# Kernel tuning notes

Hardware: AMD Instinct MI355X
Metric: run time of the kernel (lower is better)

The kernel has to match this reference:

```python
import jax, jax.numpy as jnp
import numpy as np
from math import factorial

NODES = 40000      # number of nodes
EDGES = 640000     # number of edges (avg degree 16)
MUL = 8            # multiplicity of each irrep in hidden (8x0e+8x1e+8x2e)
NB = 16            # radial basis size (radial_neurons[0])
MAXR = 3.0         # max_radius
NSPECIES = 8
DEG = 16.0         # num_neighbors normalization
R8 = 1.0 / np.sqrt(8.0)

# ---------- real Clebsch-Gordan coefficients (precomputed with numpy) ----------
def _clebsch(j1, m1, j2, m2, j3, m3):
    f = factorial
    if m1 + m2 != m3:
        return 0.0
    pref = ((2*j3+1) * f(j3+j1-j2) * f(j3-j1+j2) * f(j1+j2-j3) / f(j1+j2+j3+1)) ** 0.5
    pref *= (f(j3+m3)*f(j3-m3)*f(j1-m1)*f(j1+m1)*f(j2-m2)*f(j2+m2)) ** 0.5
    lo = max(0, j2-j3-m1, j1-j3+m2)
    hi = min(j1+j2-j3, j1-m1, j2+m2)
    s = 0.0
    for k in range(lo, hi+1):
        s += (-1)**k / (f(k)*f(j1+j2-j3-k)*f(j1-m1-k)*f(j2+m2-k)*f(j3-j2+m1+k)*f(j3-j1-m2+k))
    return pref * s

def _U(l):
    # complex -> real spherical-harmonic change of basis (rows: real m, cols: complex m)
    U = np.zeros((2*l+1, 2*l+1), dtype=complex)
    s2 = 2 ** -0.5
    for m in range(-l, l+1):
        if m > 0:
            U[m+l, m+l] = (-1)**m * s2; U[m+l, -m+l] = s2
        elif m == 0:
            U[l, l] = 1.0
        else:
            U[m+l, m+l] = 1j*s2; U[m+l, -m+l] = -1j*((-1)**m)*s2
    return U

def _real_cg(l1, l2, l3):
    C = np.zeros((2*l1+1, 2*l2+1, 2*l3+1))
    for m1 in range(-l1, l1+1):
        for m2 in range(-l2, l2+1):
            m3 = m1 + m2
            if abs(m3) <= l3:
                C[m1+l1, m2+l2, m3+l3] = _clebsch(l1, m1, l2, m2, l3, m3)
    T = np.einsum('am,bn,co,mno->abc', _U(l1).conj(), _U(l2).conj(), _U(l3), C)
    R = T.imag if np.abs(T.imag).max() > np.abs(T.real).max() else T.real
    return jnp.asarray(R.astype(np.float32))

PATHS = [(0,0,0),(0,1,1),(0,2,2),(1,0,1),(1,1,0),(1,1,1),(1,1,2),
         (1,2,1),(1,2,2),(2,0,2),(2,1,1),(2,1,2),(2,2,0),(2,2,1),(2,2,2)]
CG = {p: _real_cg(*p) for p in PATHS}
NIN = {0: 3.0, 1: 6.0, 2: 6.0}  # fan-in path counts per output l in hidden convs

# ---------- irrep feature layout: [.., 72] = 8x0e | 8x1e | 8x2e ----------
def _split(h):
    lead = h.shape[:-1]
    return (h[..., :MUL],
            h[..., MUL:4*MUL].reshape(lead + (MUL, 3)),
            h[..., 4*MUL:].reshape(lead + (MUL, 5)))

def _merge(s, v, t):
    lead = s.shape[:-1]
    return jnp.concatenate([s, v.reshape(lead + (3*MUL,)), t.reshape(lead + (5*MUL,))], -1)

def _act(h):
    # e3nn Activation: silu on 0e scalars, identity on l>0
    s, v, t = _split(h)
    return _merge(jax.nn.silu(s), v, t)

def _radial(emb, w1, b1, w2, b2):
    return jax.nn.silu(emb @ w1 + b1) @ w2 + b2

def _sh(u):
    # component-normalized real spherical harmonics l=0,1,2 of unit vectors u [E,3]
    x, y, z = u[:, 0], u[:, 1], u[:, 2]
    c15 = np.sqrt(15.0); c5 = np.sqrt(5.0); c3 = np.sqrt(3.0)
    y1 = jnp.stack([y, z, x], -1) * c3
    y2 = jnp.stack([c15*x*y, c15*y*z, 0.5*c5*(3*z*z - 1.0), c15*x*z, 0.5*c15*(x*x - y*y)], -1)
    return jnp.concatenate([jnp.ones_like(x)[:, None], y1, y2], -1)

def _soft_onehot(r):
    # e3nn soft_one_hot_linspace, basis='smooth_finite', cutoff=True
    values = jnp.linspace(0.0, MAXR, NB + 2)[1:-1]
    step = MAXR / (NB + 1)
    d = (r[:, None] - values) / step
    inside = jnp.abs(d) < 1.0
    dd = jnp.where(inside, d, 0.0)
    f = jnp.exp(-1.0 / (1.0 + dd)) * jnp.exp(-1.0 / (1.0 - dd))
    return 1.14136 * np.exp(2.0) * jnp.where(inside, f, 0.0)

def _tp_first(hs, sh, w):
    # uvu TP: 8x0e (x) SH(1x0e+1x1e+1x2e) -> hidden; hs [E,8], sh [E,9], w [E,3,8]
    m_s = w[:, 0] * hs * sh[:, :1]
    m_v = w[:, 1][..., None] * hs[..., None] * sh[:, None, 1:4]
    m_t = w[:, 2][..., None] * hs[..., None] * sh[:, None, 4:9]
    return _merge(m_s, m_v, m_t)

def _tp_uuu(h1, h2, w):
    # depthwise (uuu) CG tensor product hidden (x) hidden -> hidden; w [E,15,8]
    s1, v1, t1 = _split(h1); s2, v2, t2 = _split(h2)
    a = {0: s1[..., None], 1: v1, 2: t1}
    b = {0: s2[..., None], 1: v2, 2: t2}
    out = {0: 0.0, 1: 0.0, 2: 0.0}
    for p, (l1, l2, l3) in enumerate(PATHS):
        out[l3] = out[l3] + w[:, p, :, None] * jnp.einsum('eci,ecj,ijk->eck', a[l1], b[l2], CG[(l1, l2, l3)])
    return _merge(out[0][..., 0] / np.sqrt(NIN[0]), out[1] / np.sqrt(NIN[1]), out[2] / np.sqrt(NIN[2]))

def _lin_hidden(h, lin):
    # irrep-wise linear self-connection, lin [3,8,8]
    s, v, t = _split(h)
    return _merge(s @ lin[0] * R8,
                  jnp.einsum('ncm,cd->ndm', v, lin[1]) * R8,
                  jnp.einsum('ncm,cd->ndm', t, lin[2]) * R8)

def _model(x, edge_index, edge_vec, embed_w, lin0, lin1, lin2, out_w,
           r0_w1, r0_b1, r0_w2, r0_b2, r1_w1, r1_b1, r1_w2, r1_b2,
           r2_w1, r2_b1, r2_w2, r2_b2):
    src, dst = edge_index[0], edge_index[1]
    h = embed_w[x]                                   # [N, 8] scalar node feats
    r = jnp.sqrt(jnp.sum(edge_vec**2, -1) + 1e-12)
    emb = _soft_onehot(r)                            # [E, 16]
    hb_sh = _sh(edge_vec / r[:, None])               # [E, 9]
    rdeg = 1.0 / np.sqrt(DEG)
    # conv 0 + activation
    w = _radial(emb, r0_w1, r0_b1, r0_w2, r0_b2).reshape(-1, 3, MUL)
    m = _tp_first(h[src], hb_sh, w)                  # [E, 72]
    agg = jax.ops.segment_sum(m, dst, num_segments=NODES) * rdeg
    h = _act(agg.at[:, :MUL].add((h @ lin0) * R8))
    hb = _act(m)
    # convs 1..2 + activation
    for (w1, b1, w2, b2, lin) in ((r1_w1, r1_b1, r1_w2, r1_b2, lin1),
                                  (r2_w1, r2_b1, r2_w2, r2_b2, lin2)):
        w = _radial(emb, w1, b1, w2, b2).reshape(-1, 15, MUL)
        m = _tp_uuu(h[src], hb, w)
        agg = jax.ops.segment_sum(m, dst, num_segments=NODES) * rdeg
        h = _act(_lin_hidden(h, lin) + agg)
        hb = _act(m)
    # output FullyConnectedTensorProduct(h, h) -> 8x0e (paths l(x)l->0)
    s, v, t = _split(h)
    i0 = s[:, :, None] * s[:, None, :]
    i1 = jnp.einsum('nim,njm->nij', v, v) / np.sqrt(3.0)
    i2 = jnp.einsum('nim,njm->nij', t, t) / np.sqrt(5.0)
    out = (jnp.einsum('nij,ijk->nk', i0, out_w[0])
           + jnp.einsum('nij,ijk->nk', i1, out_w[1])
           + jnp.einsum('nij,ijk->nk', i2, out_w[2])) / np.sqrt(3.0 * MUL * MUL)
    return out

def setup_inputs() -> dict:
    key = jax.random.key(0)
    ks = jax.random.split(key, 16)
    inp = {}
    inp['x'] = jax.random.randint(ks[0], (NODES,), 0, NSPECIES)
    inp['edge_index'] = jax.random.randint(ks[1], (2, EDGES), 0, NODES)
    inp['edge_vec'] = jax.random.normal(ks[2], (EDGES, 3), dtype=jnp.float32)
    inp['embed_w'] = jax.random.normal(ks[3], (NSPECIES, MUL), dtype=jnp.float32)
    inp['lin0'] = jax.random.normal(ks[4], (MUL, MUL), dtype=jnp.float32)
    inp['lin1'] = jax.random.normal(ks[5], (3, MUL, MUL), dtype=jnp.float32)
    inp['lin2'] = jax.random.normal(ks[6], (3, MUL, MUL), dtype=jnp.float32)
    inp['out_w'] = jax.random.normal(ks[7], (3, MUL, MUL, MUL), dtype=jnp.float32)
    for i, (name, od) in enumerate((('r0', 3*MUL), ('r1', 15*MUL), ('r2', 15*MUL))):
        k1, k2 = jax.random.split(ks[8+i])
        inp[name+'_w1'] = jax.random.normal(k1, (NB, 64), dtype=jnp.float32) / np.sqrt(NB)
        inp[name+'_b1'] = jnp.zeros((64,), dtype=jnp.float32)
        inp[name+'_w2'] = jax.random.normal(k2, (64, od), dtype=jnp.float32) / 8.0
        inp[name+'_b2'] = jnp.zeros((od,), dtype=jnp.float32)
    return inp

def reference(x, edge_index, edge_vec, embed_w, lin0, lin1, lin2, out_w,
              r0_w1, r0_b1, r0_w2, r0_b2, r1_w1, r1_b1, r1_w2, r1_b2,
              r2_w1, r2_b1, r2_w2, r2_b2):
    return _model(x, edge_index, edge_vec, embed_w, lin0, lin1, lin2, out_w,
                  r0_w1, r0_b1, r0_w2, r0_b2, r1_w1, r1_b1, r1_w2, r1_b2,
                  r2_w1, r2_b1, r2_w2, r2_b2)
```

## Files before the change

kernel.cpp:

```cpp
#include <hip/hip_runtime.h>

#define NODES 40000
#define EDGES 640000

typedef float f32x2v __attribute__((ext_vector_type(2)));
typedef float f32x4v __attribute__((ext_vector_type(4)));
typedef short short8v __attribute__((ext_vector_type(8)));

__device__ __forceinline__ float silu_f(float x) { return x / (1.0f + __expf(-x)); }
__device__ __forceinline__ f32x2v mk2(float a, float b) { f32x2v r; r[0] = a; r[1] = b; return r; }

__device__ __forceinline__ void tp_uuu2(const f32x2v* wv,
                                        f32x2v as, const f32x2v* av, const f32x2v* at,
                                        f32x2v bs, const f32x2v* bv, const f32x2v* bt,
                                        f32x2v& ms, f32x2v* mv, f32x2v* mt)
{
    const float CR = 0.70710678f;
    const float K1 = 0.31622777f;
    const float K3 = 0.54772256f;
    const float KA = 0.40824829f;
    const float KB = 0.70710678f;
    const float KC = 0.81649658f;
    const float L4 = 0.63245553f;
    const float G2 = 0.53452248f;
    const float G1 = 0.26726124f;
    const float HH = 0.46291005f;

    f32x2v os = {0.f, 0.f};
    f32x2v ov0 = {0.f, 0.f}, ov1 = {0.f, 0.f}, ov2 = {0.f, 0.f};
    f32x2v ot0 = {0.f, 0.f}, ot1 = {0.f, 0.f}, ot2 = {0.f, 0.f};
    f32x2v ot3 = {0.f, 0.f}, ot4 = {0.f, 0.f};

    os += wv[0] * as * bs;
    ov0 += wv[1] * as * bv[0]; ov1 += wv[1] * as * bv[1]; ov2 += wv[1] * as * bv[2];
    ot0 += wv[2] * as * bt[0]; ot1 += wv[2] * as * bt[1]; ot2 += wv[2] * as * bt[2];
    ot3 += wv[2] * as * bt[3]; ot4 += wv[2] * as * bt[4];
    ov0 += wv[3] * av[0] * bs; ov1 += wv[3] * av[1] * bs; ov2 += wv[3] * av[2] * bs;
    os += wv[4] * (-0.57735027f) * (av[0]*bv[0] + av[1]*bv[1] + av[2]*bv[2]);
    ov0 += wv[5] * CR * (av[1]*bv[2] - av[2]*bv[1]);
    ov1 += wv[5] * CR * (av[2]*bv[0] - av[0]*bv[2]);
    ov2 += wv[5] * CR * (av[0]*bv[1] - av[1]*bv[0]);
    ot0 += wv[6] * CR * (av[2]*bv[0] + av[0]*bv[2]);
    ot1 += wv[6] * CR * (av[0]*bv[1] + av[1]*bv[0]);
    ot2 += wv[6] * 0.40824829f * (2.f*av[1]*bv[1] - av[2]*bv[2] - av[0]*bv[0]);
    ot3 += wv[6] * CR * (av[2]*bv[1] + av[1]*bv[2]);
    ot4 += wv[6] * CR * (av[2]*bv[2] - av[0]*bv[0]);
    ov0 += wv[7] * (-K3*av[1]*bt[1] + K1*av[0]*bt[2] - K3*av[2]*bt[0] + K3*av[0]*bt[4]);
    ov1 += wv[7] * (-2.f*K1*av[1]*bt[2] - K3*av[2]*bt[3] - K3*av[0]*bt[1]);
    ov2 += wv[7] * (-K3*av[1]*bt[3] + K1*av[2]*bt[2] - K3*av[0]*bt[0] - K3*av[2]*bt[4]);
    ot0 += wv[8] * ( KC*av[1]*bt[4] - KA*av[2]*bt[3] + KA*av[0]*bt[1]);
    ot1 += wv[8] * ( KA*av[1]*bt[3] - KB*av[2]*bt[2] - KA*av[0]*bt[0] - KA*av[2]*bt[4]);
    ot2 += wv[8] * ( KB*av[2]*bt[1] - KB*av[0]*bt[3]);
    ot3 += wv[8] * (-KA*av[1]*bt[1] + KB*av[0]*bt[2] + KA*av[2]*bt[0] - KA*av[0]*bt[4]);
    ot4 += wv[8] * (-KC*av[1]*bt[0] + KA*av[2]*bt[1] + KA*av[0]*bt[3]);
    ot0 += wv[9] * at[0] * bs; ot1 += wv[9] * at[1] * bs; ot2 += wv[9] * at[2] * bs;
    ot3 += wv[9] * at[3] * bs; ot4 += wv[9] * at[4] * bs;
    ov0 += wv[10] * (-K3*bv[1]*at[1] + K1*bv[0]*at[2] - K3*bv[2]*at[0] + K3*bv[0]*at[4]);
    ov1 += wv[10] * (-2.f*K1*bv[1]*at[2] - K3*bv[2]*at[3] - K3*bv[0]*at[1]);
    ov2 += wv[10] * (-K3*bv[1]*at[3] + K1*bv[2]*at[2] - K3*bv[0]*at[0] - K3*bv[2]*at[4]);
    ot0 -= wv[11] * ( KC*bv[1]*at[4] - KA*bv[2]*at[3] + KA*bv[0]*at[1]);
    ot1 -= wv[11] * ( KA*bv[1]*at[3] - KB*bv[2]*at[2] - KA*bv[0]*at[0] - KA*bv[2]*at[4]);
    ot2 -= wv[11] * ( KB*bv[2]*at[1] - KB*bv[0]*at[3]);
    ot3 -= wv[11] * (-KA*bv[1]*at[1] + KB*bv[0]*at[2] + KA*bv[2]*at[0] - KA*bv[0]*at[4]);
    ot4 -= wv[11] * (-KC*bv[1]*at[0] + KA*bv[2]*at[1] + KA*bv[0]*at[3]);
    os += wv[12] * 0.44721360f * (at[0]*bt[0] + at[1]*bt[1] + at[2]*bt[2] + at[3]*bt[3] + at[4]*bt[4]);
    ov0 += wv[13] * ( K1*(at[0]*bt[1] - at[1]*bt[0]) + K3*(at[3]*bt[2] - at[2]*bt[3]) + K1*(at[4]*bt[3] - at[3]*bt[4]) );
    ov1 += wv[13] * ( L4*(at[0]*bt[4] - at[4]*bt[0]) + K1*(at[1]*bt[3] - at[3]*bt[1]) );
    ov2 += wv[13] * ( K1*(at[3]*bt[0] - at[0]*bt[3]) + K3*(at[2]*bt[1] - at[1]*bt[2]) + K1*(at[4]*bt[1] - at[1]*bt[4]) );
    ot0 += wv[14] * ( G2*(at[2]*bt[0] + at[0]*bt[2]) - HH*(at[1]*bt[3] + at[3]*bt[1]) );
    ot1 += wv[14] * (-HH*(at[3]*bt[0] + at[0]*bt[3]) + HH*(at[1]*bt[4] + at[4]*bt[1]) - G1*(at[2]*bt[1] + at[1]*bt[2]) );
    ot2 += wv[14] * ( G2*(at[0]*bt[0] + at[4]*bt[4] - at[2]*bt[2]) - G1*(at[1]*bt[1] + at[3]*bt[3]) );
    ot3 += wv[14] * (-HH*(at[1]*bt[0] + at[0]*bt[1]) - HH*(at[3]*bt[4] + at[4]*bt[3]) - G1*(at[2]*bt[3] + at[3]*bt[2]) );
    ot4 += wv[14] * ( G2*(at[2]*bt[4] + at[4]*bt[2]) + HH*(at[1]*bt[1] - at[3]*bt[3]) );

    ms = os * 0.57735027f;
    mv[0] = ov0 * 0.40824829f; mv[1] = ov1 * 0.40824829f; mv[2] = ov2 * 0.40824829f;
    mt[0] = ot0 * 0.40824829f; mt[1] = ot1 * 0.40824829f; mt[2] = ot2 * 0.40824829f;
    mt[3] = ot3 * 0.40824829f; mt[4] = ot4 * 0.40824829f;
}

__global__ void deg_kernel(const int* __restrict__ eidx, int* __restrict__ deg)
{
    int e = blockIdx.x * 256 + threadIdx.x;
    if (e < EDGES) atomicAdd(&deg[eidx[EDGES + e]], 1);
}

__launch_bounds__(1024)
__global__ void scan_kernel(const int* __restrict__ deg, int* __restrict__ off,
                            int* __restrict__ cursor)
{
    __shared__ int part[1024];
    const int t = threadIdx.x;
    const int base = t * 40;
    int v[40];
    if (t < 1000) {
        const int4* p4 = (const int4*)(deg + base);
        #pragma unroll
        for (int i = 0; i < 10; ++i) {
            int4 q = p4[i];
            v[4 * i + 0] = q.x; v[4 * i + 1] = q.y;
            v[4 * i + 2] = q.z; v[4 * i + 3] = q.w;
        }
    } else {
        #pragma unroll
        for (int i = 0; i < 40; ++i) v[i] = 0;
    }
    int loc[40];
    int s = 0;
    #pragma unroll
    for (int i = 0; i < 40; ++i) { loc[i] = s; s += v[i]; }
    part[t] = s;
    __syncthreads();
    for (int d = 1; d < 1024; d <<= 1) {
        int vv = (t >= d) ? part[t - d] : 0;
        __syncthreads();
        part[t] += vv;
        __syncthreads();
    }
    int tb = (t == 0) ? 0 : part[t - 1];
    if (t < 1000) {
        #pragma unroll
        for (int i = 0; i < 40; ++i) {
            off[base + i] = tb + loc[i];
            cursor[base + i] = tb + loc[i];
        }
    }
    if (t == 1023) off[NODES] = part[1023];
}

__global__ void build_kernel(const int* __restrict__ eidx, const float* __restrict__ ev,
                             int* __restrict__ cursor,
                             float* __restrict__ evp, int* __restrict__ srcs)
{
    int e = blockIdx.x * 256 + threadIdx.x;
    if (e < EDGES) {
        int dst = eidx[EDGES + e];
        int p = atomicAdd(&cursor[dst], 1);
        srcs[p] = eidx[e];
        evp[p * 3 + 0] = ev[e * 3 + 0];
        evp[p * 3 + 1] = ev[e * 3 + 1];
        evp[p * 3 + 2] = ev[e * 3 + 2];
    }
}

__launch_bounds__(256, 3)
__global__ void layer0_edge(const float* __restrict__ evp, const int* __restrict__ srcs,
                            const int* __restrict__ xs, const float* __restrict__ embw,
                            const float* __restrict__ w1, const float* __restrict__ b1,
                            const float* __restrict__ w2, const float* __restrict__ b2,
                            float* __restrict__ mbuf)
{
    __shared__ float emb_s[128 * 17];
    __shared__ float hid_s[128 * 68];
    __shared__ float w2t[24 * 68];
    const int tid = threadIdx.x;
    const int e0 = blockIdx.x * 128;

    for (int idx = tid; idx < 64 * 24; idx += 256) {
        int j = idx / 24, o = idx - j * 24;
        w2t[o * 68 + j] = w2[idx];
    }
    for (int idx = tid; idx < 2048; idx += 256) {
        int e = idx >> 4, i = idx & 15;
        const float* ep = evp + (size_t)(e0 + e) * 3;
        float ex = ep[0], ey = ep[1], ez = ep[2];
        float r = sqrtf(ex * ex + ey * ey + ez * ez + 1e-12f);
        float d = r * (17.0f / 3.0f) - (float)(i + 1);
        float f = 0.0f;
        if (fabsf(d) < 1.0f) f = 8.433572869f * __expf(-2.0f / (1.0f - d * d));
        emb_s[e * 17 + i] = f;
    }
    __syncthreads();

    {
        const int egp = tid >> 3;
        const int jb = (tid & 7) * 8;
        float acc2[4][8];
        #pragma unroll
        for (int el = 0; el < 4; ++el)
            #pragma unroll
            for (int k = 0; k < 8; ++k) acc2[el][k] = b1[jb + k];
        #pragma unroll
        for (int i = 0; i < 16; ++i) {
            float4 wa = *(const float4*)&w1[i * 64 + jb];
            float4 wb = *(const float4*)&w1[i * 64 + jb + 4];
            #pragma unroll
            for (int el = 0; el < 4; ++el) {
                float evv = emb_s[(egp * 4 + el) * 17 + i];
                acc2[el][0] += evv * wa.x; acc2[el][1] += evv * wa.y;
                acc2[el][2] += evv * wa.z; acc2[el][3] += evv * wa.w;
                acc2[el][4] += evv * wb.x; acc2[el][5] += evv * wb.y;
                acc2[el][6] += evv * wb.z; acc2[el][7] += evv * wb.w;
            }
        }
        #pragma unroll
        for (int el = 0; el < 4; ++el)
            #pragma unroll
            for (int k = 0; k < 8; ++k)
                hid_s[(egp * 4 + el) * 68 + jb + k] = silu_f(acc2[el][k]);
    }
    __syncthreads();

    const int c = tid & 7, g = (tid >> 3) & 7, wv_ = tid >> 6;
    float wacc[3][4];
    #pragma unroll
    for (int p = 0; p < 3; ++p) {
        float bb = b2[p * 8 + c];
        #pragma unroll
        for (int q = 0; q < 4; ++q) wacc[p][q] = bb;
    }
    for (int jb = 0; jb < 64; jb += 4) {
        float4 h4[4];
        #pragma unroll
        for (int q = 0; q < 4; ++q)
            h4[q] = *(const float4*)&hid_s[(wv_ * 32 + q * 8 + g) * 68 + jb];
        #pragma unroll
        for (int p = 0; p < 3; ++p) {
            float4 w4 = *(const float4*)&w2t[(p * 8 + c) * 68 + jb];
            #pragma unroll
            for (int q = 0; q < 4; ++q)
                wacc[p][q] += h4[q].x * w4.x + h4[q].y * w4.y + h4[q].z * w4.z + h4[q].w * w4.w;
        }
    }

    const int ebase = wv_ * 32 + g;
    const float c3 = 1.7320508f, c15 = 3.8729833f, c5 = 2.2360680f;
    #pragma unroll
    for (int q = 0; q < 4; ++q) {
        const int sl = e0 + ebase + 8 * q;
        const int sn = srcs[sl];
        float hs = embw[xs[sn] * 8 + c];
        const float* ep = evp + (size_t)sl * 3;
        float ex = ep[0], ey = ep[1], ez = ep[2];
        float r = sqrtf(ex * ex + ey * ey + ez * ez + 1e-12f);
        float inv = 1.0f / r;
        float x = ex * inv, y = ey * inv, z = ez * inv;

        float* me = mbuf + (size_t)sl * 72 + c * 9;
        me[0] = wacc[0][q] * hs;
        me[1] = wacc[1][q] * hs * (c3 * y);
        me[2] = wacc[1][q] * hs * (c3 * z);
        me[3] = wacc[1][q] * hs * (c3 * x);
        me[4] = wacc[2][q] * hs * (c15 * x * y);
        me[5] = wacc[2][q] * hs * (c15 * y * z);
        me[6] = wacc[2][q] * hs * (0.5f * c5 * (3.f * z * z - 1.f));
        me[7] = wacc[2][q] * hs * (c15 * x * z);
        me[8] = wacc[2][q] * hs * (0.5f * c15 * (x * x - y * y));
    }
}

__launch_bounds__(256, 2)
__global__ void tp_edge(const float* __restrict__ evp, const int* __restrict__ srcs,
                        const float* __restrict__ h,
                        const float* __restrict__ w1, const float* __restrict__ b1,
                        const float* __restrict__ w2, const float* __restrict__ b2,
                        float* __restrict__ mbuf)
{
    __shared__ float ws_t[120 * 132];
    __shared__ unsigned short hid_s[128 * 64];
    float* emb_s = ws_t;

    const int tid = threadIdx.x;
    const int e0 = blockIdx.x * 128;

    for (int idx = tid; idx < 2048; idx += 256) {
        int e = idx >> 4, i = idx & 15;
        const float* ep = evp + (size_t)(e0 + e) * 3;
        float ex = ep[0], ey = ep[1], ez = ep[2];
        float r = sqrtf(ex * ex + ey * ey + ez * ez + 1e-12f);
        float d = r * (17.0f / 3.0f) - (float)(i + 1);
        float f = 0.0f;
        if (fabsf(d) < 1.0f) f = 8.433572869f * __expf(-2.0f / (1.0f - d * d));
        emb_s[e * 17 + i] = f;
    }
    __syncthreads();

    {
        const int egp = tid >> 3;
        const int jb = (tid & 7) * 8;
        f32x2v acc2[2][8];
        #pragma unroll
        for (int pr = 0; pr < 2; ++pr)
            #pragma unroll
            for (int k = 0; k < 8; ++k) { float bb = b1[jb + k]; acc2[pr][k] = mk2(bb, bb); }
        #pragma unroll
        for (int i = 0; i < 16; ++i) {
            float4 wa = *(const float4*)&w1[i * 64 + jb];
            float4 wb = *(const float4*)&w1[i * 64 + jb + 4];
            #pragma unroll
            for (int pr = 0; pr < 2; ++pr) {
                f32x2v evv = mk2(emb_s[(egp * 4 + 2 * pr) * 17 + i],
                                 emb_s[(egp * 4 + 2 * pr + 1) * 17 + i]);
                acc2[pr][0] += evv * wa.x; acc2[pr][1] += evv * wa.y;
                acc2[pr][2] += evv * wa.z; acc2[pr][3] += evv * wa.w;
                acc2[pr][4] += evv * wb.x; acc2[pr][5] += evv * wb.y;
                acc2[pr][6] += evv * wb.z; acc2[pr][7] += evv * wb.w;
            }
        }
        #pragma unroll
        for (int pr = 0; pr < 2; ++pr) {
            #pragma unroll
            for (int u = 0; u < 2; ++u) {
                unsigned int us[8];
                #pragma unroll
                for (int k = 0; k < 8; ++k) {
                    unsigned int b = __float_as_uint(silu_f(acc2[pr][k][u]));
                    b += 0x7fffu + ((b >> 16) & 1u);
                    us[k] = b >> 16;
                }
                uint4 pk;
                pk.x = us[0] | (us[1] << 16);
                pk.y = us[2] | (us[3] << 16);
                pk.z = us[4] | (us[5] << 16);
                pk.w = us[6] | (us[7] << 16);
                int rr = egp * 4 + 2 * pr + u;
                *(uint4*)&hid_s[rr * 64 + (jb ^ ((rr & 7) << 3))] = pk;
            }
        }
    }
    __syncthreads();

    {
        const int l  = tid & 63;
        const int wq = tid >> 6;
        const int lr = l & 15;
        const int lg = l >> 4;

        short8v bhi[2][2], blo[2][2];
        #pragma unroll
        for (int n2 = 0; n2 < 2; ++n2) {
            int col  = (2 * wq + n2) * 16 + lr;
            int colc = col < 120 ? col : 119;
            #pragma unroll
            for (int ks = 0; ks < 2; ++ks) {
                short8v hv, lv;
                #pragma unroll
                for (int j = 0; j < 8; ++j) {
                    int k = ks * 32 + lg * 8 + j;
                    float v = w2[k * 120 + colc];
                    if (col >= 120) v = 0.0f;
                    unsigned bb = __float_as_uint(v);
                    unsigned rh = bb + 0x7fffu + ((bb >> 16) & 1u);
                    float hf = __uint_as_float((rh >> 16) << 16);
                    unsigned bl = __float_as_uint(v - hf);
                    bl += 0x7fffu + ((bl >> 16) & 1u);
                    hv[j] = (short)(rh >> 16);
                    lv[j] = (short)(bl >> 16);
                }
                bhi[n2][ks] = hv;
                blo[n2][ks] = lv;
            }
        }

        for (int m = 0; m < 8; ++m) {
            int e  = 16 * m + lr;
            int sw = (e & 7) << 3;
            short8v a0 = *(const short8v*)&hid_s[e * 64 + ((lg * 8) ^ sw)];
            short8v a1 = *(const short8v*)&hid_s[e * 64 + ((32 + lg * 8) ^ sw)];
            #pragma unroll
            for (int n2 = 0; n2 < 2; ++n2) {
                int col = (2 * wq + n2) * 16 + lr;
                float bias = (col < 120) ? b2[col] : 0.0f;
                f32x4v acc;
                acc[0] = bias; acc[1] = bias; acc[2] = bias; acc[3] = bias;
                acc = __builtin_amdgcn_mfma_f32_16x16x32_bf16(a0, bhi[n2][0], acc, 0, 0, 0);
                acc = __builtin_amdgcn_mfma_f32_16x16x32_bf16(a1, bhi[n2][1], acc, 0, 0, 0);
                acc = __builtin_amdgcn_mfma_f32_16x16x32_bf16(a0, blo[n2][0], acc, 0, 0, 0);
                acc = __builtin_amdgcn_mfma_f32_16x16x32_bf16(a1, blo[n2][1], acc, 0, 0, 0);
                if (col < 120)
                    *(f32x4v*)&ws_t[col * 132 + 16 * m + lg * 4] = acc;
            }
        }
    }
    __syncthreads();

    const int c = tid & 7, g = (tid >> 3) & 7, wv_ = tid >> 6;
    const int ebase = wv_ * 32 + g;
    int sn[4];
    #pragma unroll
    for (int q = 0; q < 4; ++q) sn[q] = srcs[e0 + ebase + 8 * q];

    #pragma unroll
    for (int hh = 0; hh < 2; ++hh) {
        const float* hn0 = h + (size_t)sn[2 * hh] * 72 + c * 9;
        const float* hn1 = h + (size_t)sn[2 * hh + 1] * 72 + c * 9;
        const float* me0 = mbuf + (size_t)(e0 + ebase + 8 * (2 * hh)) * 72 + c * 9;
        const float* me1 = mbuf + (size_t)(e0 + ebase + 8 * (2 * hh + 1)) * 72 + c * 9;

        f32x2v as = mk2(hn0[0], hn1[0]);
        f32x2v av[3], at[5], bv[3], bt[5];
        #pragma unroll
        for (int i = 0; i < 3; ++i) av[i] = mk2(hn0[1 + i], hn1[1 + i]);
        #pragma unroll
        for (int i = 0; i < 5; ++i) at[i] = mk2(hn0[4 + i], hn1[4 + i]);
        f32x2v bs = mk2(silu_f(me0[0]), silu_f(me1[0]));
        #pragma unroll
        for (int i = 0; i < 3; ++i) bv[i] = mk2(me0[1 + i], me1[1 + i]);
        #pragma unroll
        for (int i = 0; i < 5; ++i) bt[i] = mk2(me0[4 + i], me1[4 + i]);

        f32x2v wvv[15];
        #pragma unroll
        for (int p = 0; p < 15; ++p)
            wvv[p] = mk2(ws_t[(p * 8 + c) * 132 + ebase + 16 * hh],
                         ws_t[(p * 8 + c) * 132 + ebase + 16 * hh + 8]);

        f32x2v ms, mv[3], mt[5];
        tp_uuu2(wvv, as, av, at, bs, bv, bt, ms, mv, mt);

        float* mo0 = mbuf + (size_t)(e0 + ebase + 8 * (2 * hh)) * 72 + c * 9;
        float* mo1 = mbuf + (size_t)(e0 + ebase + 8 * (2 * hh + 1)) * 72 + c * 9;
        mo0[0] = ms[0]; mo1[0] = ms[1];
        #pragma unroll
        for (int i = 0; i < 3; ++i) { mo0[1 + i] = mv[i][0]; mo1[1 + i] = mv[i][1]; }
        #pragma unroll
        for (int i = 0; i < 5; ++i) { mo0[4 + i] = mt[i][0]; mo1[4 + i] = mt[i][1]; }
    }
}

__global__ void node0(const int* __restrict__ xs, const float* __restrict__ embw,
                      const float* __restrict__ lin0, const float* __restrict__ mbuf,
                      const int* __restrict__ off, float* __restrict__ h)
{
    int idx = blockIdx.x * 256 + threadIdx.x;
    int n = idx >> 3, c = idx & 7;
    int xb = xs[n] * 8;
    float dot = 0.f;
    #pragma unroll
    for (int d = 0; d < 8; ++d) dot += embw[xb + d] * lin0[d * 8 + c];

    float an[9];
    #pragma unroll
    for (int i = 0; i < 9; ++i) an[i] = 0.f;
    const int beg = off[n], end = off[n + 1];
    for (int p = beg; p < end; ++p) {
        const float* me = mbuf + (size_t)p * 72 + c * 9;
        #pragma unroll
        for (int i = 0; i < 9; ++i) an[i] += me[i];
    }

    float* hn = h + (size_t)n * 72 + c * 9;
    hn[0] = silu_f(an[0] * 0.25f + dot * 0.35355339f);
    #pragma unroll
    for (int i = 1; i < 9; ++i) hn[i] = an[i] * 0.25f;
}

__global__ void node12(const float* __restrict__ hin, const float* __restrict__ lin,
                       const float* __restrict__ mbuf, const int* __restrict__ off,
                       float* __restrict__ hout)
{
    int idx = blockIdx.x * 256 + threadIdx.x;
    int n = idx >> 3, d = idx & 7;

    float an[9];
    #pragma unroll
    for (int i = 0; i < 9; ++i) an[i] = 0.f;
    const int beg = off[n], end = off[n + 1];
    for (int p = beg; p < end; ++p) {
        const float* me = mbuf + (size_t)p * 72 + d * 9;
        #pragma unroll
        for (int i = 0; i < 9; ++i) an[i] += me[i];
    }

    const float* hn = hin + (size_t)n * 72;
    float* ho = hout + (size_t)n * 72 + d * 9;

    float s = 0.f;
    #pragma unroll
    for (int c = 0; c < 8; ++c) s += hn[c * 9] * lin[c * 8 + d];
    ho[0] = silu_f(s * 0.35355339f + an[0] * 0.25f);
    #pragma unroll
    for (int i = 0; i < 3; ++i) {
        float v = 0.f;
        #pragma unroll
        for (int c = 0; c < 8; ++c) v += hn[c * 9 + 1 + i] * lin[64 + c * 8 + d];
        ho[1 + i] = v * 0.35355339f + an[1 + i] * 0.25f;
    }
    #pragma unroll
    for (int i = 0; i < 5; ++i) {
        float t = 0.f;
        #pragma unroll
        for (int c = 0; c < 8; ++c) t += hn[c * 9 + 4 + i] * lin[128 + c * 8 + d];
        ho[4 + i] = t * 0.35355339f + an[4 + i] * 0.25f;
    }
}

__global__ void node12_out(const float* __restrict__ hin, const float* __restrict__ lin,
                           const float* __restrict__ mbuf, const int* __restrict__ off,
                           const float* __restrict__ outw, float* __restrict__ out)
{
    __shared__ float hrec[32][72];
    int idx = blockIdx.x * 256 + threadIdx.x;
    int n = idx >> 3, d = idx & 7;
    int nl = threadIdx.x >> 3;

    float an[9];
    #pragma unroll
    for (int i = 0; i < 9; ++i) an[i] = 0.f;
    const int beg = off[n], end = off[n + 1];
    for (int p = beg; p < end; ++p) {
        const float* me = mbuf + (size_t)p * 72 + d * 9;
        #pragma unroll
        for (int i = 0; i < 9; ++i) an[i] += me[i];
    }

    const float* hn = hin + (size_t)n * 72;
    float* ho = &hrec[nl][d * 9];

    float s = 0.f;
    #pragma unroll
    for (int c = 0; c < 8; ++c) s += hn[c * 9] * lin[c * 8 + d];
    ho[0] = silu_f(s * 0.35355339f + an[0] * 0.25f);
    #pragma unroll
    for (int i = 0; i < 3; ++i) {
        float v = 0.f;
        #pragma unroll
        for (int c = 0; c < 8; ++c) v += hn[c * 9 + 1 + i] * lin[64 + c * 8 + d];
        ho[1 + i] = v * 0.35355339f + an[1 + i] * 0.25f;
    }
    #pragma unroll
    for (int i = 0; i < 5; ++i) {
        float t = 0.f;
        #pragma unroll
        for (int c = 0; c < 8; ++c) t += hn[c * 9 + 4 + i] * lin[128 + c * 8 + d];
        ho[4 + i] = t * 0.35355339f + an[4 + i] * 0.25f;
    }
    __syncthreads();

    const float* hr = &hrec[nl][0];
    float sv[8], vv[24], tv[40];
    #pragma unroll
    for (int i = 0; i < 8; ++i) {
        sv[i] = hr[i * 9];
        #pragma unroll
        for (int q = 0; q < 3; ++q) vv[i * 3 + q] = hr[i * 9 + 1 + q];
        #pragma unroll
        for (int q = 0; q < 5; ++q) tv[i * 5 + q] = hr[i * 9 + 4 + q];
    }
    float acc = 0.f;
    #pragma unroll
    for (int i = 0; i < 8; ++i) {
        #pragma unroll
        for (int j = 0; j < 8; ++j) {
            float dv = vv[i*3+0]*vv[j*3+0] + vv[i*3+1]*vv[j*3+1] + vv[i*3+2]*vv[j*3+2];
            float dt = tv[i*5+0]*tv[j*5+0] + tv[i*5+1]*tv[j*5+1] + tv[i*5+2]*tv[j*5+2]
                     + tv[i*5+3]*tv[j*5+3] + tv[i*5+4]*tv[j*5+4];
            int o = (i * 8 + j) * 8 + d;
            acc += sv[i] * sv[j] * outw[o]
                 + dv * 0.57735027f * outw[512 + o]
                 + dt * 0.44721360f * outw[1024 + o];
        }
    }
    out[n * 8 + d] = acc * 0.072168784f;
}

extern "C" void kernel_launch(void* const* d_in, const int* in_sizes, int n_in,
                              void* d_out, int out_size, void* d_ws, size_t ws_size,
                              hipStream_t stream)
{
    const int*   x    = (const int*)  d_in[0];
    const int*   eidx = (const int*)  d_in[1];
    const float* ev   = (const float*)d_in[2];
    const float* embw = (const float*)d_in[3];
    const float* lin0 = (const float*)d_in[4];
    const float* lin1 = (const float*)d_in[5];
    const float* lin2 = (const float*)d_in[6];
    const float* outw = (const float*)d_in[7];
    const float* r0w1 = (const float*)d_in[8];
    const float* r0b1 = (const float*)d_in[9];
    const float* r0w2 = (const float*)d_in[10];
    const float* r0b2 = (const float*)d_in[11];
    const float* r1w1 = (const float*)d_in[12];
    const float* r1b1 = (const float*)d_in[13];
    const float* r1w2 = (const float*)d_in[14];
    const float* r1b2 = (const float*)d_in[15];
    const float* r2w1 = (const float*)d_in[16];
    const float* r2b1 = (const float*)d_in[17];
    const float* r2w2 = (const float*)d_in[18];
    const float* r2b2 = (const float*)d_in[19];

    float* mbuf = (float*)d_ws;
    float* hA   = mbuf + (size_t)EDGES * 72;
    float* hB   = hA + (size_t)NODES * 72;
    float* evp  = hB + (size_t)NODES * 72;
    int*   deg    = (int*)(evp + (size_t)EDGES * 3);
    int*   off    = deg + NODES;
    int*   cursor = off + NODES + 1;
    int*   srcs   = cursor + NODES;

    const int EBI = (EDGES + 255) / 256;
    const int EB  = EDGES / 128;
    const int NBK = NODES * 8 / 256;

    hipMemsetAsync(deg, 0, NODES * sizeof(int), stream);
    deg_kernel<<<EBI, 256, 0, stream>>>(eidx, deg);
    scan_kernel<<<1, 1024, 0, stream>>>(deg, off, cursor);
    build_kernel<<<EBI, 256, 0, stream>>>(eidx, ev, cursor, evp, srcs);

    layer0_edge<<<EB, 256, 0, stream>>>(evp, srcs, x, embw, r0w1, r0b1, r0w2, r0b2, mbuf);
    node0<<<NBK, 256, 0, stream>>>(x, embw, lin0, mbuf, off, hA);

    tp_edge<<<EB, 256, 0, stream>>>(evp, srcs, hA, r1w1, r1b1, r1w2, r1b2, mbuf);
    node12<<<NBK, 256, 0, stream>>>(hA, lin1, mbuf, off, hB);

    tp_edge<<<EB, 256, 0, stream>>>(evp, srcs, hB, r2w1, r2b1, r2w2, r2b2, mbuf);
    node12_out<<<NBK, 256, 0, stream>>>(hB, lin2, mbuf, off, outw, (float*)d_out);
}
```

Baseline: 749.0 us.

## Split tp_edge weight stage into two halves to shrink LDS and raise occupancy

The radial second-layer MFMA output buffer is halved by processing the 128-edge block in two 64-edge halves. Each half's weights are computed into LDS and then consumed by the tensor-product stage before the next half starts. This cuts shared memory per block from about 80KB to about 49KB, and launch bounds are raised to 3 blocks per CU for more latency hiding. In exchange it adds an extra barrier per half and tightens the register budget, which risks spills.

```diff
diff --git a/kernel.cpp b/kernel.cpp
--- a/kernel.cpp
+++ b/kernel.cpp
@@ -249,14 +249,14 @@
     }
 }
 
-__launch_bounds__(256, 2)
+__launch_bounds__(256, 3)
 __global__ void tp_edge(const float* __restrict__ evp, const int* __restrict__ srcs,
                         const float* __restrict__ h,
                         const float* __restrict__ w1, const float* __restrict__ b1,
                         const float* __restrict__ w2, const float* __restrict__ b2,
                         float* __restrict__ mbuf)
 {
-    __shared__ float ws_t[120 * 132];
+    __shared__ float ws_t[120 * 68];
     __shared__ unsigned short hid_s[128 * 64];
     float* emb_s = ws_t;
 
@@ -320,40 +320,45 @@
     }
     __syncthreads();
 
-    {
-        const int l  = tid & 63;
-        const int wq = tid >> 6;
-        const int lr = l & 15;
-        const int lg = l >> 4;
-
-        short8v bhi[2][2], blo[2][2];
-        #pragma unroll
-        for (int n2 = 0; n2 < 2; ++n2) {
-            int col  = (2 * wq + n2) * 16 + lr;
-            int colc = col < 120 ? col : 119;
-            #pragma unroll
-            for (int ks = 0; ks < 2; ++ks) {
-                short8v hv, lv;
-                #pragma unroll
-                for (int j = 0; j < 8; ++j) {
-                    int k = ks * 32 + lg * 8 + j;
-                    float v = w2[k * 120 + colc];
-                    if (col >= 120) v = 0.0f;
-                    unsigned bb = __float_as_uint(v);
-                    unsigned rh = bb + 0x7fffu + ((bb >> 16) & 1u);
-                    float hf = __uint_as_float((rh >> 16) << 16);
-                    unsigned bl = __float_as_uint(v - hf);
-                    bl += 0x7fffu + ((bl >> 16) & 1u);
-                    hv[j] = (short)(rh >> 16);
-                    lv[j] = (short)(bl >> 16);
-                }
-                bhi[n2][ks] = hv;
-                blo[n2][ks] = lv;
+    const int l  = tid & 63;
+    const int wq = tid >> 6;
+    const int lr = l & 15;
+    const int lg = l >> 4;
+
+    short8v bhi[2][2], blo[2][2];
+    #pragma unroll
+    for (int n2 = 0; n2 < 2; ++n2) {
+        int col  = (2 * wq + n2) * 16 + lr;
+        int colc = col < 120 ? col : 119;
+        #pragma unroll
+        for (int ks = 0; ks < 2; ++ks) {
+            short8v hv, lv;
+            #pragma unroll
+            for (int j = 0; j < 8; ++j) {
+                int k = ks * 32 + lg * 8 + j;
+                float v = w2[k * 120 + colc];
+                if (col >= 120) v = 0.0f;
+                unsigned bb = __float_as_uint(v);
+                unsigned rh = bb + 0x7fffu + ((bb >> 16) & 1u);
+                float hf = __uint_as_float((rh >> 16) << 16);
+                unsigned bl = __float_as_uint(v - hf);
+                bl += 0x7fffu + ((bl >> 16) & 1u);
+                hv[j] = (short)(rh >> 16);
+                lv[j] = (short)(bl >> 16);
             }
-        }
-
-        for (int m = 0; m < 8; ++m) {
-            int e  = 16 * m + lr;
+            bhi[n2][ks] = hv;
+            blo[n2][ks] = lv;
+        }
+    }
+
+    const int c = tid & 7, g = (tid >> 3) & 7, wv_ = tid >> 6;
+    const int ebh = wv_ * 16 + g;
+
+    #pragma unroll
+    for (int half = 0; half < 2; ++half) {
+        #pragma unroll
+        for (int mm = 0; mm < 4; ++mm) {
+            int e  = 64 * half + 16 * mm + lr;
             int sw = (e & 7) << 3;
             short8v a0 = *(const short8v*)&hid_s[e * 64 + ((lg * 8) ^ sw)];
             short8v a1 = *(const short8v*)&hid_s[e * 64 + ((32 + lg * 8) ^ sw)];
@@ -368,53 +373,50 @@
                 acc = __builtin_amdgcn_mfma_f32_16x16x32_bf16(a0, blo[n2][0], acc, 0, 0, 0);
                 acc = __builtin_amdgcn_mfma_f32_16x16x32_bf16(a1, blo[n2][1], acc, 0, 0, 0);
                 if (col < 120)
-                    *(f32x4v*)&ws_t[col * 132 + 16 * m + lg * 4] = acc;
+                    *(f32x4v*)&ws_t[col * 68 + 16 * mm + lg * 4] = acc;
             }
         }
-    }
-    __syncthreads();
-
-    const int c = tid & 7, g = (tid >> 3) & 7, wv_ = tid >> 6;
-    const int ebase = wv_ * 32 + g;
-    int sn[4];
-    #pragma unroll
-    for (int q = 0; q < 4; ++q) sn[q] = srcs[e0 + ebase + 8 * q];
-
-    #pragma unroll
-    for (int hh = 0; hh < 2; ++hh) {
-        const float* hn0 = h + (size_t)sn[2 * hh] * 72 + c * 9;
-        const float* hn1 = h + (size_t)sn[2 * hh + 1] * 72 + c * 9;
-        const float* me0 = mbuf + (size_t)(e0 + ebase + 8 * (2 * hh)) * 72 + c * 9;
-        const float* me1 = mbuf + (size_t)(e0 + ebase + 8 * (2 * hh + 1)) * 72 + c * 9;
-
-        f32x2v as = mk2(hn0[0], hn1[0]);
-        f32x2v av[3], at[5], bv[3], bt[5];
-        #pragma unroll
-        for (int i = 0; i < 3; ++i) av[i] = mk2(hn0[1 + i], hn1[1 + i]);
-        #pragma unroll
-        for (int i = 0; i < 5; ++i) at[i] = mk2(hn0[4 + i], hn1[4 + i]);
-        f32x2v bs = mk2(silu_f(me0[0]), silu_f(me1[0]));
-        #pragma unroll
-        for (int i = 0; i < 3; ++i) bv[i] = mk2(me0[1 + i], me1[1 + i]);
-        #pragma unroll
-        for (int i = 0; i < 5; ++i) bt[i] = mk2(me0[4 + i], me1[4 + i]);
-
-        f32x2v wvv[15];
-        #pragma unroll
-        for (int p = 0; p < 15; ++p)
-            wvv[p] = mk2(ws_t[(p * 8 + c) * 132 + ebase + 16 * hh],
-                         ws_t[(p * 8 + c) * 132 + ebase + 16 * hh + 8]);
-
-        f32x2v ms, mv[3], mt[5];
-        tp_uuu2(wvv, as, av, at, bs, bv, bt, ms, mv, mt);
-
-        float* mo0 = mbuf + (size_t)(e0 + ebase + 8 * (2 * hh)) * 72 + c * 9;
-        float* mo1 = mbuf + (size_t)(e0 + ebase + 8 * (2 * hh + 1)) * 72 + c * 9;
-        mo0[0] = ms[0]; mo1[0] = ms[1];
-        #pragma unroll
-        for (int i = 0; i < 3; ++i) { mo0[1 + i] = mv[i][0]; mo1[1 + i] = mv[i][1]; }
-        #pragma unroll
-        for (int i = 0; i < 5; ++i) { mo0[4 + i] = mt[i][0]; mo1[4 + i] = mt[i][1]; }
+        __syncthreads();
+
+        {
+            const int eA = e0 + 64 * half + ebh;
+            const int eB = eA + 8;
+            const int snA = srcs[eA], snB = srcs[eB];
+            const float* hn0 = h + (size_t)snA * 72 + c * 9;
+            const float* hn1 = h + (size_t)snB * 72 + c * 9;
+            const float* me0 = mbuf + (size_t)eA * 72 + c * 9;
+            const float* me1 = mbuf + (size_t)eB * 72 + c * 9;
+
+            f32x2v as = mk2(hn0[0], hn1[0]);
+            f32x2v av[3], at[5], bv[3], bt[5];
+            #pragma unroll
+            for (int i = 0; i < 3; ++i) av[i] = mk2(hn0[1 + i], hn1[1 + i]);
+            #pragma unroll
+            for (int i = 0; i < 5; ++i) at[i] = mk2(hn0[4 + i], hn1[4 + i]);
+            f32x2v bs = mk2(silu_f(me0[0]), silu_f(me1[0]));
+            #pragma unroll
+            for (int i = 0; i < 3; ++i) bv[i] = mk2(me0[1 + i], me1[1 + i]);
+            #pragma unroll
+            for (int i = 0; i < 5; ++i) bt[i] = mk2(me0[4 + i], me1[4 + i]);
+
+            f32x2v wvv[15];
+            #pragma unroll
+            for (int p = 0; p < 15; ++p)
+                wvv[p] = mk2(ws_t[(p * 8 + c) * 68 + ebh],
+                             ws_t[(p * 8 + c) * 68 + ebh + 8]);
+
+            f32x2v ms, mv[3], mt[5];
+            tp_uuu2(wvv, as, av, at, bs, bv, bt, ms, mv, mt);
+
+            float* mo0 = mbuf + (size_t)eA * 72 + c * 9;
+            float* mo1 = mbuf + (size_t)eB * 72 + c * 9;
+            mo0[0] = ms[0]; mo1[0] = ms[1];
+            #pragma unroll
+            for (int i = 0; i < 3; ++i) { mo0[1 + i] = mv[i][0]; mo1[1 + i] = mv[i][1]; }
+            #pragma unroll
+            for (int i = 0; i < 5; ++i) { mo0[4 + i] = mt[i][0]; mo1[4 + i] = mt[i][1]; }
+        }
+        if (half == 0) __syncthreads();
     }
 }
 
```

Result: faster. 680.7 us (-9.1%).
